# Performance work log

Hardware: AMD Instinct MI355X
Metric: run time of the kernel (lower is better)

Reference implementation:

```python
import jax, jax.numpy as jnp
import numpy as np

SUB_NO = 32
HID = 16
BATCH = 64
T = 2048


def setup_inputs() -> dict:
    key = jax.random.key(0)
    ks = jax.random.split(key, 7)
    return {
        "input_data": jax.random.normal(ks[0], (BATCH, T, SUB_NO), jnp.float32),
        "W_hif": jax.random.normal(ks[1], (SUB_NO, HID), jnp.float32) * 0.01,
        "W_hin": jax.random.normal(ks[2], (SUB_NO, HID), jnp.float32) * 0.01,
        "W_hhf": jax.random.normal(ks[3], (SUB_NO, HID, HID), jnp.float32) * 0.01,
        "W_hhn": jax.random.normal(ks[4], (SUB_NO, HID, HID), jnp.float32) * 0.01,
        "bias_hi": jax.random.normal(ks[5], (SUB_NO * 2 * HID,), jnp.float32) * 0.01,
        "bias_hh": jax.random.normal(ks[6], (SUB_NO * 2 * HID,), jnp.float32) * 0.01,
    }


def reference(input_data, W_hif, W_hin, W_hhf, W_hhn, bias_hi, bias_hh):
    B, T_, S = input_data.shape
    H = W_hif.shape[1]
    # Bias layout matches torch: first S*H rows = forget gate, last S*H = new gate,
    # contiguous per-subunit blocks of size H.
    b_if = bias_hi[: S * H].reshape(S, H)
    b_in = bias_hi[S * H :].reshape(S, H)
    b_hf = bias_hh[: S * H].reshape(S, H)
    b_hn = bias_hh[S * H :].reshape(S, H)

    def step(h, x_t):
        # h: [B, S, H], x_t: [B, S] (scalar input per subunit)
        i_f = x_t[:, :, None] * W_hif + b_if
        i_n = x_t[:, :, None] * W_hin + b_in
        # Block-diagonal recurrence: each subunit has its own HxH matrix.
        h_f = jnp.einsum("shk,bsk->bsh", W_hhf, h) + b_hf
        h_n = jnp.einsum("shk,bsk->bsh", W_hhn, h) + b_hn
        f = jax.nn.sigmoid(i_f + h_f)
        n = jnp.tanh(i_n + f * h_n)
        h_new = f * n + (1.0 - f) * h
        return h_new, h_new

    h0 = jnp.zeros((B, S, H), input_data.dtype)
    xs = jnp.swapaxes(input_data, 0, 1)  # [T, B, S]
    _, ys = jax.lax.scan(step, h0, xs)  # ys: [T, B, S, H]
    return jnp.transpose(ys, (1, 0, 2, 3)).reshape(B, T_, S * H)
```

## Files before the change

kernel.cpp:

```cpp
#include <hip/hip_runtime.h>


#define TT 2048
#define SS 32
#define HH 16

template <int R>
__device__ __forceinline__ void bcast_ror(int hi, float* u) {
    u[R] = __int_as_float(
        __builtin_amdgcn_update_dpp(hi, hi, 0x120 + R, 0xF, 0xF, false));
    if constexpr (R + 1 < 16) bcast_ror<R + 1>(hi, u);
}

template <int R>
__device__ __forceinline__ void probe_ror(int jj, int* k) {
    k[R] = __builtin_amdgcn_update_dpp(jj, jj, 0x120 + R, 0xF, 0xF, false);
    if constexpr (R + 1 < 16) probe_ror<R + 1>(jj, k);
}

template <bool REFILL>
__device__ __forceinline__ void block16(
    float& h, float& omh, float (&xbuf)[16],
    const float* xq, float* opq,
    const float (&wf)[16], const float (&wn)[16],
    float wifp, float winp, float bfp, float binp, float bhnp)
{
    float hs[16];
#pragma unroll
    for (int p = 0; p < 16; ++p) {
        const float x = xbuf[p];
        if constexpr (REFILL) xbuf[p] = xq[p * SS];

        float u[16];
        u[0] = h;
        bcast_ror<1>(__float_as_int(h), u);

        float a0 = __builtin_fmaf(x, wifp, bfp), a1 = 0.0f, a2 = 0.0f, a3 = 0.0f;
        float c0 = bhnp, c1 = 0.0f, c2 = 0.0f, c3 = 0.0f;
#pragma unroll
        for (int kk = 0; kk < 4; ++kk) {
            a0 = __builtin_fmaf(wf[4*kk+0], u[4*kk+0], a0);
            a1 = __builtin_fmaf(wf[4*kk+1], u[4*kk+1], a1);
            a2 = __builtin_fmaf(wf[4*kk+2], u[4*kk+2], a2);
            a3 = __builtin_fmaf(wf[4*kk+3], u[4*kk+3], a3);
            c0 = __builtin_fmaf(wn[4*kk+0], u[4*kk+0], c0);
            c1 = __builtin_fmaf(wn[4*kk+1], u[4*kk+1], c1);
            c2 = __builtin_fmaf(wn[4*kk+2], u[4*kk+2], c2);
            c3 = __builtin_fmaf(wn[4*kk+3], u[4*kk+3], c3);
        }
        const float accf = (a0 + a1) + (a2 + a3);
        const float accn = (c0 + c1) + (c2 + c3);

        const float f   = __builtin_amdgcn_rcpf(1.0f + __builtin_amdgcn_exp2f(accf));
        const float inp = __builtin_fmaf(x, winp, binp);
        const float y   = __builtin_fmaf(f, accn, inp);
        const float rr  = __builtin_amdgcn_rcpf(1.0f + __builtin_amdgcn_exp2f(y));
        const float nmh = __builtin_fmaf(-2.0f, rr, omh);
        h   = __builtin_fmaf(f, nmh, h);
        omh = 1.0f - h;

        asm volatile("v_mov_b32 %0, %1" : "=v"(hs[p]) : "v"(h));
        opq[(size_t)p * (SS * HH)] = hs[p];
    }
    asm volatile("" ::
        "v"(hs[0]),  "v"(hs[1]),  "v"(hs[2]),  "v"(hs[3]),
        "v"(hs[4]),  "v"(hs[5]),  "v"(hs[6]),  "v"(hs[7]),
        "v"(hs[8]),  "v"(hs[9]),  "v"(hs[10]), "v"(hs[11]),
        "v"(hs[12]), "v"(hs[13]), "v"(hs[14]), "v"(hs[15]));
}

__global__ __launch_bounds__(64) void mgu_kernel(
    const float* __restrict__ input,
    const float* __restrict__ W_hif,
    const float* __restrict__ W_hin,
    const float* __restrict__ W_hhf,
    const float* __restrict__ W_hhn,
    const float* __restrict__ bias_hi,
    const float* __restrict__ bias_hh,
    float* __restrict__ out)
{
    const int lane = threadIdx.x;
    const int sl   = lane >> 4;
    const int b    = blockIdx.x & 63;
    const int sg   = blockIdx.x >> 6;
    const int s    = sg * 4 + sl;
    const int j    = lane & 15;
    const int row  = s * HH + j;

    const float NL2E = -1.442695041f;
    const float TL2E =  2.885390082f;

    int kidx[16];
    kidx[0] = j;
    probe_ror<1>(j, kidx);

    float wf[16], wn[16];
    {
        const float* Wfr = W_hhf + row * HH;
        const float* Wnr = W_hhn + row * HH;
#pragma unroll
        for (int r = 0; r < 16; ++r) {
            wf[r] = Wfr[kidx[r]] * NL2E;
            wn[r] = Wnr[kidx[r]] * TL2E;
        }
    }
    const float wifp = W_hif[row] * NL2E;
    const float winp = W_hin[row] * TL2E;
    const float bfp  = (bias_hi[row] + bias_hh[row]) * NL2E;
    const float binp = bias_hi[SS * HH + row] * TL2E;
    const float bhnp = bias_hh[SS * HH + row] * TL2E;

    const float* xp = input + (size_t)b * (TT * SS) + s;
    float*       op = out   + (size_t)b * (TT * SS * HH) + sg * 64 + lane;

    float xbuf[16];
#pragma unroll
    for (int i = 0; i < 16; ++i) xbuf[i] = xp[i * SS];

    float h = 0.0f, omh = 1.0f;

#pragma unroll 1
    for (int t = 0; t < TT - 16; t += 16) {
        block16<true>(h, omh, xbuf,
                      xp + (size_t)(t + 16) * SS,
                      op + (size_t)t * (SS * HH),
                      wf, wn, wifp, winp, bfp, binp, bhnp);
    }
    block16<false>(h, omh, xbuf,
                   xp,
                   op + (size_t)(TT - 16) * (SS * HH),
                   wf, wn, wifp, winp, bfp, binp, bhnp);
}

extern "C" void kernel_launch(void* const* d_in, const int* in_sizes, int n_in,
                              void* d_out, int out_size, void* d_ws, size_t ws_size,
                              hipStream_t stream) {
    const float* input   = (const float*)d_in[0];
    const float* W_hif   = (const float*)d_in[1];
    const float* W_hin   = (const float*)d_in[2];
    const float* W_hhf   = (const float*)d_in[3];
    const float* W_hhn   = (const float*)d_in[4];
    const float* bias_hi = (const float*)d_in[5];
    const float* bias_hh = (const float*)d_in[6];
    float* out = (float*)d_out;

    mgu_kernel<<<dim3(512), dim3(64), 0, stream>>>(
        input, W_hif, W_hin, W_hhf, W_hhn, bias_hi, bias_hh, out);
}
```

Measured before the change: 561.5 us.

## Interleave two batch recurrences per wavefront to expose instruction-level parallelism

Each wavefront now advances two independent batch elements' recurrences in lockstep, and the grid is halved to 256 blocks. The serial per-step latency chain (DPP broadcasts, FMAs, exp/rcp) of one sequence can overlap with the other's. The cost is half as many wavefronts, so fewer SIMDs are occupied, plus higher register pressure from the duplicated buffers.

After: 765.9 us. +36.4%, slower.

```diff
diff --git a/kernel.cpp b/kernel.cpp
--- a/kernel.cpp
+++ b/kernel.cpp
@@ -19,54 +19,77 @@
 }
 
 template <bool REFILL>
-__device__ __forceinline__ void block16(
-    float& h, float& omh, float (&xbuf)[16],
-    const float* xq, float* opq,
+__device__ __forceinline__ void block16_dual(
+    float (&h)[2], float (&omh)[2],
+    float (&xb0)[16], float (&xb1)[16],
+    const float* xq0, const float* xq1,
+    float* op0, float* op1,
     const float (&wf)[16], const float (&wn)[16],
     float wifp, float winp, float bfp, float binp, float bhnp)
 {
-    float hs[16];
+    float hs0[16], hs1[16];
 #pragma unroll
     for (int p = 0; p < 16; ++p) {
-        const float x = xbuf[p];
-        if constexpr (REFILL) xbuf[p] = xq[p * SS];
+        const float x0 = xb0[p];
+        const float x1 = xb1[p];
+        if constexpr (REFILL) {
+            xb0[p] = xq0[p * SS];
+            xb1[p] = xq1[p * SS];
+        }
 
-        float u[16];
-        u[0] = h;
-        bcast_ror<1>(__float_as_int(h), u);
+        float u[2][16];
+        u[0][0] = h[0];
+        u[1][0] = h[1];
+        bcast_ror<1>(__float_as_int(h[0]), u[0]);
+        bcast_ror<1>(__float_as_int(h[1]), u[1]);
 
-        float a0 = __builtin_fmaf(x, wifp, bfp), a1 = 0.0f, a2 = 0.0f, a3 = 0.0f;
-        float c0 = bhnp, c1 = 0.0f, c2 = 0.0f, c3 = 0.0f;
+        const float xx[2] = {x0, x1};
+        float accf[2], accn[2];
 #pragma unroll
-        for (int kk = 0; kk < 4; ++kk) {
-            a0 = __builtin_fmaf(wf[4*kk+0], u[4*kk+0], a0);
-            a1 = __builtin_fmaf(wf[4*kk+1], u[4*kk+1], a1);
-            a2 = __builtin_fmaf(wf[4*kk+2], u[4*kk+2], a2);
-            a3 = __builtin_fmaf(wf[4*kk+3], u[4*kk+3], a3);
-            c0 = __builtin_fmaf(wn[4*kk+0], u[4*kk+0], c0);
-            c1 = __builtin_fmaf(wn[4*kk+1], u[4*kk+1], c1);
-            c2 = __builtin_fmaf(wn[4*kk+2], u[4*kk+2], c2);
-            c3 = __builtin_fmaf(wn[4*kk+3], u[4*kk+3], c3);
+        for (int i = 0; i < 2; ++i) {
+            float a0 = __builtin_fmaf(xx[i], wifp, bfp), a1 = 0.f, a2 = 0.f, a3 = 0.f;
+            float c0 = bhnp, c1 = 0.f, c2 = 0.f, c3 = 0.f;
+#pragma unroll
+            for (int kk = 0; kk < 4; ++kk) {
+                a0 = __builtin_fmaf(wf[4*kk+0], u[i][4*kk+0], a0);
+                a1 = __builtin_fmaf(wf[4*kk+1], u[i][4*kk+1], a1);
+                a2 = __builtin_fmaf(wf[4*kk+2], u[i][4*kk+2], a2);
+                a3 = __builtin_fmaf(wf[4*kk+3], u[i][4*kk+3], a3);
+                c0 = __builtin_fmaf(wn[4*kk+0], u[i][4*kk+0], c0);
+                c1 = __builtin_fmaf(wn[4*kk+1], u[i][4*kk+1], c1);
+                c2 = __builtin_fmaf(wn[4*kk+2], u[i][4*kk+2], c2);
+                c3 = __builtin_fmaf(wn[4*kk+3], u[i][4*kk+3], c3);
+            }
+            accf[i] = (a0 + a1) + (a2 + a3);
+            accn[i] = (c0 + c1) + (c2 + c3);
         }
-        const float accf = (a0 + a1) + (a2 + a3);
-        const float accn = (c0 + c1) + (c2 + c3);
 
-        const float f   = __builtin_amdgcn_rcpf(1.0f + __builtin_amdgcn_exp2f(accf));
-        const float inp = __builtin_fmaf(x, winp, binp);
-        const float y   = __builtin_fmaf(f, accn, inp);
-        const float rr  = __builtin_amdgcn_rcpf(1.0f + __builtin_amdgcn_exp2f(y));
-        const float nmh = __builtin_fmaf(-2.0f, rr, omh);
-        h   = __builtin_fmaf(f, nmh, h);
-        omh = 1.0f - h;
+#pragma unroll
+        for (int i = 0; i < 2; ++i) {
+            const float f   = __builtin_amdgcn_rcpf(1.0f + __builtin_amdgcn_exp2f(accf[i]));
+            const float inp = __builtin_fmaf(xx[i], winp, binp);
+            const float y   = __builtin_fmaf(f, accn[i], inp);
+            const float rr  = __builtin_amdgcn_rcpf(1.0f + __builtin_amdgcn_exp2f(y));
+            const float nmh = __builtin_fmaf(-2.0f, rr, omh[i]);
+            h[i]   = __builtin_fmaf(f, nmh, h[i]);
+            omh[i] = 1.0f - h[i];
+        }
 
-        asm volatile("v_mov_b32 %0, %1" : "=v"(hs[p]) : "v"(h));
-        opq[(size_t)p * (SS * HH)] = hs[p];
+        asm volatile("v_mov_b32 %0, %1" : "=v"(hs0[p]) : "v"(h[0]));
+        asm volatile("v_mov_b32 %0, %1" : "=v"(hs1[p]) : "v"(h[1]));
+        op0[(size_t)p * (SS * HH)] = hs0[p];
+        op1[(size_t)p * (SS * HH)] = hs1[p];
     }
     asm volatile("" ::
-        "v"(hs[0]),  "v"(hs[1]),  "v"(hs[2]),  "v"(hs[3]),
-        "v"(hs[4]),  "v"(hs[5]),  "v"(hs[6]),  "v"(hs[7]),
-        "v"(hs[8]),  "v"(hs[9]),  "v"(hs[10]), "v"(hs[11]),
-        "v"(hs[12]), "v"(hs[13]), "v"(hs[14]), "v"(hs[15]));
+        "v"(hs0[0]),  "v"(hs0[1]),  "v"(hs0[2]),  "v"(hs0[3]),
+        "v"(hs0[4]),  "v"(hs0[5]),  "v"(hs0[6]),  "v"(hs0[7]),
+        "v"(hs0[8]),  "v"(hs0[9]),  "v"(hs0[10]), "v"(hs0[11]),
+        "v"(hs0[12]), "v"(hs0[13]), "v"(hs0[14]), "v"(hs0[15]));
+    asm volatile("" ::
+        "v"(hs1[0]),  "v"(hs1[1]),  "v"(hs1[2]),  "v"(hs1[3]),
+        "v"(hs1[4]),  "v"(hs1[5]),  "v"(hs1[6]),  "v"(hs1[7]),
+        "v"(hs1[8]),  "v"(hs1[9]),  "v"(hs1[10]), "v"(hs1[11]),
+        "v"(hs1[12]), "v"(hs1[13]), "v"(hs1[14]), "v"(hs1[15]));
 }
 
 __global__ __launch_bounds__(64) void mgu_kernel(
@@ -81,10 +104,11 @@
 {
     const int lane = threadIdx.x;
     const int sl   = lane >> 4;
-    const int b    = blockIdx.x & 63;
-    const int sg   = blockIdx.x >> 6;
+    const int j    = lane & 15;
+    const int bA   = blockIdx.x & 31;
+    const int bB   = bA + 32;
+    const int sg   = blockIdx.x >> 5;
     const int s    = sg * 4 + sl;
-    const int j    = lane & 15;
     const int row  = s * HH + j;
 
     const float NL2E = -1.442695041f;
@@ -110,26 +134,35 @@
     const float binp = bias_hi[SS * HH + row] * TL2E;
     const float bhnp = bias_hh[SS * HH + row] * TL2E;
 
-    const float* xp = input + (size_t)b * (TT * SS) + s;
-    float*       op = out   + (size_t)b * (TT * SS * HH) + sg * 64 + lane;
+    const float* xpA = input + (size_t)bA * (TT * SS) + s;
+    const float* xpB = input + (size_t)bB * (TT * SS) + s;
+    float*       opA = out   + (size_t)bA * (TT * SS * HH) + sg * 64 + lane;
+    float*       opB = out   + (size_t)bB * (TT * SS * HH) + sg * 64 + lane;
 
-    float xbuf[16];
+    float xbA[16], xbB[16];
 #pragma unroll
-    for (int i = 0; i < 16; ++i) xbuf[i] = xp[i * SS];
+    for (int i = 0; i < 16; ++i) {
+        xbA[i] = xpA[i * SS];
+        xbB[i] = xpB[i * SS];
+    }
 
-    float h = 0.0f, omh = 1.0f;
+    float h[2]   = {0.0f, 0.0f};
+    float omh[2] = {1.0f, 1.0f};
 
 #pragma unroll 1
     for (int t = 0; t < TT - 16; t += 16) {
-        block16<true>(h, omh, xbuf,
-                      xp + (size_t)(t + 16) * SS,
-                      op + (size_t)t * (SS * HH),
-                      wf, wn, wifp, winp, bfp, binp, bhnp);
+        block16_dual<true>(h, omh, xbA, xbB,
+                           xpA + (size_t)(t + 16) * SS,
+                           xpB + (size_t)(t + 16) * SS,
+                           opA + (size_t)t * (SS * HH),
+                           opB + (size_t)t * (SS * HH),
+                           wf, wn, wifp, winp, bfp, binp, bhnp);
     }
-    block16<false>(h, omh, xbuf,
-                   xp,
-                   op + (size_t)(TT - 16) * (SS * HH),
-                   wf, wn, wifp, winp, bfp, binp, bhnp);
+    block16_dual<false>(h, omh, xbA, xbB,
+                        xpA, xpB,
+                        opA + (size_t)(TT - 16) * (SS * HH),
+                        opB + (size_t)(TT - 16) * (SS * HH),
+                        wf, wn, wifp, winp, bfp, binp, bhnp);
 }
 
 extern "C" void kernel_launch(void* const* d_in, const int* in_sizes, int n_in,
@@ -144,6 +177,6 @@
     const float* bias_hh = (const float*)d_in[6];
     float* out = (float*)d_out;
 
-    mgu_kernel<<<dim3(512), dim3(64), 0, stream>>>(
+    mgu_kernel<<<dim3(256), dim3(64), 0, stream>>>(
         input, W_hif, W_hin, W_hhf, W_hhn, bias_hi, bias_hh, out);
 }
```
